# Optimization experiments

Hardware: AMD Instinct MI355X
Metric: run time of the kernel (lower is better)

Reference implementation:

```python
import jax, jax.numpy as jnp
import numpy as np
import math

DIM = 1024
HEADS = 16
DH = DIM // HEADS
HIDDEN = 4 * DIM
B, N = 2, 1024
DT = 0.05


def _cplx(r, i):
    return jax.lax.complex(r, i)


def clin(x, Wr, Wi, br, bi):
    # complex linear: (xr + i xi)(Wr + i Wi)^T + (br + i bi)
    xr, xi = x.real, x.imag
    real = xr @ Wr.T - xi @ Wi.T + br
    imag = xr @ Wi.T + xi @ Wr.T + bi
    return _cplx(real, imag)


def setup_inputs() -> dict:
    key = jax.random.key(0)
    ks = jax.random.split(key, 32)
    s = 0.02
    d = {
        'x_real': jax.random.normal(ks[0], (B, N, DIM), jnp.float32),
        'x_imag': jax.random.normal(ks[1], (B, N, DIM), jnp.float32),
    }
    i = 2
    for name in ['q', 'k', 'v', 'o']:
        d[f'Wr_{name}'] = jax.random.normal(ks[i], (DIM, DIM), jnp.float32) * s; i += 1
        d[f'Wi_{name}'] = jax.random.normal(ks[i], (DIM, DIM), jnp.float32) * s; i += 1
        d[f'br_{name}'] = jnp.zeros((DIM,), jnp.float32)
        d[f'bi_{name}'] = jnp.zeros((DIM,), jnp.float32)
    d['Wr_f1'] = jax.random.normal(ks[i], (HIDDEN, DIM), jnp.float32) * s; i += 1
    d['Wi_f1'] = jax.random.normal(ks[i], (HIDDEN, DIM), jnp.float32) * s; i += 1
    d['br_f1'] = jnp.zeros((HIDDEN,), jnp.float32)
    d['bi_f1'] = jnp.zeros((HIDDEN,), jnp.float32)
    d['Wr_f2'] = jax.random.normal(ks[i], (DIM, HIDDEN), jnp.float32) * s; i += 1
    d['Wi_f2'] = jax.random.normal(ks[i], (DIM, HIDDEN), jnp.float32) * s; i += 1
    d['br_f2'] = jnp.zeros((DIM,), jnp.float32)
    d['bi_f2'] = jnp.zeros((DIM,), jnp.float32)
    H0 = jax.random.normal(ks[i], (DIM, DIM), jnp.float32) * s; i += 1
    d['H'] = (H0 + H0.T) / 2
    d['dt'] = jnp.float32(DT)
    return d


def _forward(x_real, x_imag,
             Wr_q, Wi_q, br_q, bi_q, Wr_k, Wi_k, br_k, bi_k,
             Wr_v, Wi_v, br_v, bi_v, Wr_o, Wi_o, br_o, bi_o,
             Wr_f1, Wi_f1, br_f1, bi_f1, Wr_f2, Wi_f2, br_f2, bi_f2,
             H, dt):
    x = _cplx(x_real, x_imag)  # [B,N,D] complex64
    scale = 1.0 / math.sqrt(DH)

    # --- Quantum Fourier attention ---
    def heads(t):
        return t.reshape(B, N, HEADS, DH).transpose(0, 2, 1, 3)  # [B,H,N,dh]
    Q = heads(clin(x, Wr_q, Wi_q, br_q, bi_q))
    K = heads(clin(x, Wr_k, Wi_k, br_k, bi_k))
    V = heads(clin(x, Wr_v, Wi_v, br_v, bi_v))
    Qf = jnp.fft.fft(Q, axis=2)
    Kf = jnp.fft.fft(K, axis=2)
    Vf = jnp.fft.fft(V, axis=2)
    scores = jnp.einsum('bhid,bhjd->bhij', Qf, jnp.conj(Kf)) * scale
    attn = jax.nn.softmax(scores.real, axis=-1).astype(jnp.complex64)
    out_f = jnp.einsum('bhij,bhjd->bhid', attn, Vf)
    out = jnp.fft.ifft(out_f, axis=2).transpose(0, 2, 1, 3).reshape(B, N, DIM)
    attn_out = clin(out, Wr_o, Wi_o, br_o, bi_o)
    x = x + attn_out

    # --- Quantum feed-forward (GELU on real & imag separately, exact erf) ---
    h = clin(x, Wr_f1, Wi_f1, br_f1, bi_f1)
    h = _cplx(jax.nn.gelu(h.real, approximate=False),
              jax.nn.gelu(h.imag, approximate=False))
    x = x + clin(h, Wr_f2, Wi_f2, br_f2, bi_f2)

    # --- Schrodinger unitary evolution: U = expm(-i H dt) ---
    A = _cplx(jnp.zeros_like(H), -(H * dt))  # complex64
    U = jax.scipy.linalg.expm(A)
    out = (x.reshape(B * N, DIM) @ U).reshape(B, N, DIM)
    return out


def reference(x_real, x_imag,
              Wr_q, Wi_q, br_q, bi_q, Wr_k, Wi_k, br_k, bi_k,
              Wr_v, Wi_v, br_v, bi_v, Wr_o, Wi_o, br_o, bi_o,
              Wr_f1, Wi_f1, br_f1, bi_f1, Wr_f2, Wi_f2, br_f2, bi_f2,
              H, dt):
    out = _forward(x_real, x_imag,
                   Wr_q, Wi_q, br_q, bi_q, Wr_k, Wi_k, br_k, bi_k,
                   Wr_v, Wi_v, br_v, bi_v, Wr_o, Wi_o, br_o, bi_o,
                   Wr_f1, Wi_f1, br_f1, bi_f1, Wr_f2, Wi_f2, br_f2, bi_f2,
                   H, dt)
    # return real/imag stacked for easy real-valued comparison: [2,B,N,D]
    return jnp.stack([out.real, out.imag], axis=0)
```

## Files before the change

### kernel.cpp

```cpp
#include <hip/hip_runtime.h>
#include <cstdint>
#include <cstddef>

typedef unsigned int u32;
typedef unsigned short u16;
typedef long long i64;

typedef __attribute__((ext_vector_type(8))) short short8;
typedef __attribute__((ext_vector_type(4))) float f32x4;
typedef __attribute__((ext_vector_type(4))) int i32x4;

__device__ __forceinline__ u16 f2bf(float f) {
  u32 u = __float_as_uint(f);
  u = (u + 0x7FFFu + ((u >> 16) & 1u)) >> 16;
  return (u16)u;
}
__device__ __forceinline__ float bf2f(u16 h) { return __uint_as_float(((u32)h) << 16); }

__device__ __forceinline__ short8 neg8(short8 v) {
  i32x4 u = __builtin_bit_cast(i32x4, v);
  u = u ^ (int)0x80008000u;
  return __builtin_bit_cast(short8, u);
}
__device__ __forceinline__ f32x4 mfma16(short8 a, short8 b, f32x4 c) {
  return __builtin_amdgcn_mfma_f32_16x16x32_bf16(a, b, c, 0, 0, 0);
}
__device__ __forceinline__ float gelu_f(float x) {
  return 0.5f * x * (1.0f + erff(x * 0.7071067811865475f));
}
__device__ __forceinline__ void gl16(const u16* g, u16* l) {
  __builtin_amdgcn_global_load_lds((const __attribute__((address_space(1))) void*)g,
                                   (__attribute__((address_space(3))) void*)l, 16, 0, 0);
}
template <int N>
__device__ __forceinline__ void wait_barrier() {
  asm volatile("s_waitcnt vmcnt(%0)\n\ts_barrier" ::"i"(N) : "memory");
}

struct GemmP {
  const u16 *Arh, *Aih, *Arl, *Ail;
  const u16 *Brh, *Bih, *Brl, *Bil;
  const float *biasr, *biasi;
  const float *Resr, *Resi;
  float *Cr32, *Ci32;
  u16 *Crh, *Cih, *Crl, *Cil;
  i64 sA1, sA2, sB1, sB2, sC1, sC2;
  int ZH;
  int M, N, K, lda, ldb, ldc;
  float alpha;
  int beta, wb32, ctrans, bias_mode, bias_period, gelu, splitB;
  float bias_scale;
};

template <int CMODE, int SPLIT, int DEEP>
__global__ __launch_bounds__(256, 2) void cgemm_kernel(GemmP p) {
  constexpr int BUFU = SPLIT ? 24576 : 12288;
  constexpr int NBUF = DEEP ? 3 : 1;
  __shared__ u16 smem[BUFU * NBUF];
  constexpr bool HAS_CI = (CMODE == 0 || CMODE == 2 || CMODE == 3);
  constexpr bool AI = (CMODE == 0 || CMODE == 3);
  constexpr bool BIc = (CMODE == 0 || CMODE == 2 || CMODE == 3);
  constexpr int LPS = 3 + (AI ? 2 : 0) + (BIc ? 1 : 0);

  const int tid = threadIdx.x, lane = tid & 63, wave = tid >> 6;
  const int lrow = lane & 15, quad = lane >> 4;
  const int m0 = blockIdx.y * 128, n0 = blockIdx.x * 64;
  const int z1 = blockIdx.z / p.ZH, z2 = blockIdx.z % p.ZH;
  const i64 zA = (i64)z1 * p.sA1 + (i64)z2 * p.sA2;
  const i64 zB = (i64)z1 * p.sB1 + (i64)z2 * p.sB2;
  const i64 zC = (i64)z1 * p.sC1 + (i64)z2 * p.sC2;
  const int l4 = lane >> 2;
  const int lc = DEEP ? ((((lane & 3) ^ ((lane >> 3) & 3))) << 3) : ((lane & 3) << 3);
  const i64 aoff0 = zA + (i64)(m0 + 32 * wave + l4) * p.lda + lc;
  const i64 aoff1 = aoff0 + (i64)16 * p.lda;
  const i64 boff = zB + (i64)(n0 + 16 * wave + l4) * p.ldb + lc;
  const int lA0 = (32 * wave) * 32, lA1 = lA0 + 512;
  const int lB0 = (16 * wave) * 32;
  const int cxw = ((lrow >> 1) & 3) << 3;

  f32x4 accR[2][4], accI[2][4];
  const f32x4 z4 = {0.f, 0.f, 0.f, 0.f};
#pragma unroll
  for (int i = 0; i < 2; ++i)
#pragma unroll
    for (int j = 0; j < 4; ++j) { accR[i][j] = z4; accI[i][j] = z4; }

  const int ktn = p.K >> 5;

  if constexpr (SPLIT && !DEEP) {
    for (int kt = 0; kt < ktn; ++kt) {
      const i64 kc = (i64)(kt << 5);
      __syncthreads();
      gl16(p.Arh + aoff0 + kc, smem + lA0);
      gl16(p.Arh + aoff1 + kc, smem + lA1);
      gl16(p.Aih + aoff0 + kc, smem + 4096 + lA0);
      gl16(p.Aih + aoff1 + kc, smem + 4096 + lA1);
      gl16(p.Arl + aoff0 + kc, smem + 8192 + lA0);
      gl16(p.Arl + aoff1 + kc, smem + 8192 + lA1);
      gl16(p.Ail + aoff0 + kc, smem + 12288 + lA0);
      gl16(p.Ail + aoff1 + kc, smem + 12288 + lA1);
      gl16(p.Brh + boff + kc, smem + 16384 + lB0);
      gl16(p.Bih + boff + kc, smem + 18432 + lB0);
      if (p.splitB) {
        gl16(p.Brl + boff + kc, smem + 20480 + lB0);
        gl16(p.Bil + boff + kc, smem + 22528 + lB0);
      }
      __syncthreads();

      short8 bRh[4], bIh[4], bRl[4], bIl[4];
#pragma unroll
      for (int j = 0; j < 4; ++j) {
        const int off = (j * 16 + lrow) * 32 + quad * 8;
        bRh[j] = *(const short8*)&smem[16384 + off];
        bIh[j] = *(const short8*)&smem[18432 + off];
        if (p.splitB) {
          bRl[j] = *(const short8*)&smem[20480 + off];
          bIl[j] = *(const short8*)&smem[22528 + off];
        }
      }
#pragma unroll
      for (int i = 0; i < 2; ++i) {
        const int off = (wave * 32 + i * 16 + lrow) * 32 + quad * 8;
        short8 aRh = *(const short8*)&smem[off];
        short8 aIh = *(const short8*)&smem[4096 + off];
        short8 aRl = *(const short8*)&smem[8192 + off];
        short8 aIl = *(const short8*)&smem[12288 + off];
        if constexpr (CMODE == 0) {
          short8 nIh = neg8(aIh), nIl = neg8(aIl);
#pragma unroll
          for (int j = 0; j < 4; ++j) {
            accR[i][j] = mfma16(aRh, bRh[j], accR[i][j]);
            accR[i][j] = mfma16(nIh, bIh[j], accR[i][j]);
            accI[i][j] = mfma16(aRh, bIh[j], accI[i][j]);
            accI[i][j] = mfma16(aIh, bRh[j], accI[i][j]);
            accR[i][j] = mfma16(aRl, bRh[j], accR[i][j]);
            accR[i][j] = mfma16(nIl, bIh[j], accR[i][j]);
            accI[i][j] = mfma16(aRl, bIh[j], accI[i][j]);
            accI[i][j] = mfma16(aIl, bRh[j], accI[i][j]);
            if (p.splitB) {
              accR[i][j] = mfma16(aRh, bRl[j], accR[i][j]);
              accR[i][j] = mfma16(nIh, bIl[j], accR[i][j]);
              accI[i][j] = mfma16(aRh, bIl[j], accI[i][j]);
              accI[i][j] = mfma16(aIh, bRl[j], accI[i][j]);
            }
          }
        } else {
#pragma unroll
          for (int j = 0; j < 4; ++j) {
            accR[i][j] = mfma16(aRh, bRh[j], accR[i][j]);
            accR[i][j] = mfma16(aIh, bIh[j], accR[i][j]);
            accR[i][j] = mfma16(aRl, bRh[j], accR[i][j]);
            accR[i][j] = mfma16(aIl, bIh[j], accR[i][j]);
            accR[i][j] = mfma16(aRh, bRl[j], accR[i][j]);
            accR[i][j] = mfma16(aIh, bIl[j], accR[i][j]);
          }
        }
      }
    }
  } else if constexpr (SPLIT && DEEP) {
    auto stageS = [&](int buf, i64 kc) {
      u16* s = smem + buf * 24576;
      gl16(p.Arh + aoff0 + kc, s + lA0);
      gl16(p.Arh + aoff1 + kc, s + lA1);
      gl16(p.Aih + aoff0 + kc, s + 4096 + lA0);
      gl16(p.Aih + aoff1 + kc, s + 4096 + lA1);
      gl16(p.Arl + aoff0 + kc, s + 8192 + lA0);
      gl16(p.Arl + aoff1 + kc, s + 8192 + lA1);
      gl16(p.Ail + aoff0 + kc, s + 12288 + lA0);
      gl16(p.Ail + aoff1 + kc, s + 12288 + lA1);
      gl16(p.Brh + boff + kc, s + 16384 + lB0);
      gl16(p.Bih + boff + kc, s + 18432 + lB0);
      if (p.splitB) {
        gl16(p.Brl + boff + kc, s + 20480 + lB0);
        gl16(p.Bil + boff + kc, s + 22528 + lB0);
      }
    };
    if (ktn > 0) stageS(0, 0);
    if (ktn > 1) stageS(1, 32);
    for (int kt = 0; kt < ktn; ++kt) {
      if (kt + 1 < ktn) {
        if (p.splitB) wait_barrier<12>(); else wait_barrier<10>();
      } else {
        wait_barrier<0>();
      }
      if (kt + 2 < ktn) stageS((kt + 2) % 3, (i64)((kt + 2) << 5));
      const u16* sb = smem + (kt % 3) * 24576;

      short8 bRh[4], bIh[4], bRl[4], bIl[4];
#pragma unroll
      for (int j = 0; j < 4; ++j) {
        const int off = (j * 16 + lrow) * 32 + (quad * 8 ^ cxw);
        bRh[j] = *(const short8*)&sb[16384 + off];
        bIh[j] = *(const short8*)&sb[18432 + off];
        if (p.splitB) {
          bRl[j] = *(const short8*)&sb[20480 + off];
          bIl[j] = *(const short8*)&sb[22528 + off];
        }
      }
#pragma unroll
      for (int i = 0; i < 2; ++i) {
        const int off = (wave * 32 + i * 16 + lrow) * 32 + (quad * 8 ^ cxw);
        short8 aRh = *(const short8*)&sb[off];
        short8 aIh = *(const short8*)&sb[4096 + off];
        short8 aRl = *(const short8*)&sb[8192 + off];
        short8 aIl = *(const short8*)&sb[12288 + off];
        if constexpr (CMODE == 0) {
          short8 nIh = neg8(aIh), nIl = neg8(aIl);
#pragma unroll
          for (int j = 0; j < 4; ++j) {
            accR[i][j] = mfma16(aRh, bRh[j], accR[i][j]);
            accR[i][j] = mfma16(nIh, bIh[j], accR[i][j]);
            accI[i][j] = mfma16(aRh, bIh[j], accI[i][j]);
            accI[i][j] = mfma16(aIh, bRh[j], accI[i][j]);
            accR[i][j] = mfma16(aRl, bRh[j], accR[i][j]);
            accR[i][j] = mfma16(nIl, bIh[j], accR[i][j]);
            accI[i][j] = mfma16(aRl, bIh[j], accI[i][j]);
            accI[i][j] = mfma16(aIl, bRh[j], accI[i][j]);
            if (p.splitB) {
              accR[i][j] = mfma16(aRh, bRl[j], accR[i][j]);
              accR[i][j] = mfma16(nIh, bIl[j], accR[i][j]);
              accI[i][j] = mfma16(aRh, bIl[j], accI[i][j]);
              accI[i][j] = mfma16(aIh, bRl[j], accI[i][j]);
            }
          }
        } else {
#pragma unroll
          for (int j = 0; j < 4; ++j) {
            accR[i][j] = mfma16(aRh, bRh[j], accR[i][j]);
            accR[i][j] = mfma16(aIh, bIh[j], accR[i][j]);
            accR[i][j] = mfma16(aRl, bRh[j], accR[i][j]);
            accR[i][j] = mfma16(aIl, bIh[j], accR[i][j]);
            accR[i][j] = mfma16(aRh, bRl[j], accR[i][j]);
            accR[i][j] = mfma16(aIh, bIl[j], accR[i][j]);
          }
        }
      }
    }
  } else {
    auto stage = [&](int buf, i64 kc) {
      u16* s = smem + buf * 12288;
      gl16(p.Arh + aoff0 + kc, s + lA0);
      gl16(p.Arh + aoff1 + kc, s + lA1);
      if constexpr (AI) {
        gl16(p.Aih + aoff0 + kc, s + 4096 + lA0);
        gl16(p.Aih + aoff1 + kc, s + 4096 + lA1);
      }
      gl16(p.Brh + boff + kc, s + 8192 + lB0);
      if constexpr (BIc) gl16(p.Bih + boff + kc, s + 10240 + lB0);
    };
    if (ktn > 0) stage(0, 0);
    if (ktn > 1) stage(1, 32);
    for (int kt = 0; kt < ktn; ++kt) {
      if (kt + 1 < ktn) wait_barrier<LPS>(); else wait_barrier<0>();
      if (kt + 2 < ktn) stage((kt + 2) % 3, (i64)((kt + 2) << 5));
      const u16* sb = smem + (kt % 3) * 12288;

      short8 bR[4], bI[4];
#pragma unroll
      for (int j = 0; j < 4; ++j) {
        const int off = (j * 16 + lrow) * 32 + (quad * 8 ^ cxw);
        bR[j] = *(const short8*)&sb[8192 + off];
        if constexpr (BIc) bI[j] = *(const short8*)&sb[10240 + off];
      }
#pragma unroll
      for (int i = 0; i < 2; ++i) {
        const int off = (wave * 32 + i * 16 + lrow) * 32 + (quad * 8 ^ cxw);
        short8 aR = *(const short8*)&sb[off];
        if constexpr (CMODE == 0) {
          short8 aI = *(const short8*)&sb[4096 + off];
          short8 nI = neg8(aI);
#pragma unroll
          for (int j = 0; j < 4; ++j) {
            accR[i][j] = mfma16(aR, bR[j], accR[i][j]);
            accR[i][j] = mfma16(nI, bI[j], accR[i][j]);
            accI[i][j] = mfma16(aR, bI[j], accI[i][j]);
            accI[i][j] = mfma16(aI, bR[j], accI[i][j]);
          }
        } else if constexpr (CMODE == 1) {
#pragma unroll
          for (int j = 0; j < 4; ++j) accR[i][j] = mfma16(aR, bR[j], accR[i][j]);
        } else if constexpr (CMODE == 2) {
#pragma unroll
          for (int j = 0; j < 4; ++j) {
            accR[i][j] = mfma16(aR, bR[j], accR[i][j]);
            accI[i][j] = mfma16(aR, bI[j], accI[i][j]);
          }
        } else {
          short8 aI = *(const short8*)&sb[4096 + off];
          short8 nI = neg8(aI);
#pragma unroll
          for (int j = 0; j < 4; ++j) {
            accR[i][j] = mfma16(aR, bR[j], accR[i][j]);
            accR[i][j] = mfma16(aI, bI[j], accR[i][j]);
            accI[i][j] = mfma16(aR, bI[j], accI[i][j]);
            accI[i][j] = mfma16(nI, bR[j], accI[i][j]);
          }
        }
      }
    }
  }

#pragma unroll
  for (int i = 0; i < 2; ++i) {
#pragma unroll
    for (int j = 0; j < 4; ++j) {
      const int gn = n0 + j * 16 + lrow;
#pragma unroll
      for (int r = 0; r < 4; ++r) {
        const int gm = m0 + wave * 32 + i * 16 + quad * 4 + r;
        const i64 idx = p.ctrans ? (zC + (i64)gn * p.ldc + gm) : (zC + (i64)gm * p.ldc + gn);
        float vr = accR[i][j][r] * p.alpha;
        float vi = 0.f;
        if (HAS_CI) vi = accI[i][j][r] * p.alpha;
        if (p.beta) {
          vr += p.Cr32[idx];
          if (HAS_CI && p.Ci32) vi += p.Ci32[idx];
        }
        if (p.bias_mode == 1) {
          vr += p.biasr[gn];
          if (HAS_CI) vi += p.biasi[gn];
        } else if (p.bias_mode == 2) {
          if ((gm % p.bias_period) == 0) {
            vr += p.biasr[gn] * p.bias_scale;
            if (HAS_CI) vi += p.biasi[gn] * p.bias_scale;
          }
        }
        if (p.Resr) vr += p.Resr[idx];
        if (HAS_CI && p.Resi) vi += p.Resi[idx];
        if (p.gelu) {
          vr = gelu_f(vr);
          if (HAS_CI) vi = gelu_f(vi);
        }
        if (p.wb32 && p.Cr32) p.Cr32[idx] = vr;
        if (p.wb32 && HAS_CI && p.Ci32) p.Ci32[idx] = vi;
        if (p.Crh) {
          const u16 hh = f2bf(vr);
          p.Crh[idx] = hh;
          if (p.Crl) p.Crl[idx] = f2bf(vr - bf2f(hh));
        }
        if (HAS_CI && p.Cih) {
          const u16 hh = f2bf(vi);
          p.Cih[idx] = hh;
          if (p.Cil) p.Cil[idx] = f2bf(vi - bf2f(hh));
        }
      }
    }
  }
}

struct CvtBatch {
  const float* src[12];
  u16* hi[12];
  u16* lo[12];
  i64 cum[13];
};
__global__ __launch_bounds__(256) void cvt_batch_kernel(CvtBatch b) {
  const i64 k = (i64)blockIdx.x * 1024 + (i64)threadIdx.x * 4;
  int s = 0;
  while (k >= b.cum[s + 1]) ++s;
  const i64 base = k - b.cum[s];
  float4 v = *(const float4*)(b.src[s] + base);
  u16* hp = b.hi[s];
  u16* lp = b.lo[s];
  ushort4 h, l;
  h.x = f2bf(v.x); l.x = f2bf(v.x - bf2f(h.x));
  h.y = f2bf(v.y); l.y = f2bf(v.y - bf2f(h.y));
  h.z = f2bf(v.z); l.z = f2bf(v.z - bf2f(h.z));
  h.w = f2bf(v.w); l.w = f2bf(v.w - bf2f(h.w));
  *(ushort4*)(hp + base) = h;
  if (lp) *(ushort4*)(lp + base) = l;
}

__global__ __launch_bounds__(256) void cvt_split_kernel(const float* in, u16* hi, u16* lo,
                                                        i64 n, const float* scale_ptr) {
  const i64 base = (i64)blockIdx.x * 1024 + (i64)threadIdx.x * 4;
  const float s = scale_ptr ? *scale_ptr : 1.0f;
#pragma unroll
  for (int e = 0; e < 4; ++e) {
    const i64 k = base + e;
    if (k < n) {
      const float v = in[k] * s;
      const u16 h = f2bf(v);
      hi[k] = h;
      if (lo) lo[k] = f2bf(v - bf2f(h));
    }
  }
}

__global__ __launch_bounds__(256) void trans_cvt_kernel(const float* in, u16* outh, u16* outl) {
  __shared__ float t[32][33];
  const int b = blockIdx.z;
  const int j0 = blockIdx.y * 32;
  const int d0 = blockIdx.x * 32;
  const int r = threadIdx.x >> 5, c = threadIdx.x & 31;
  const float* ip = in + (i64)b * 1048576;
#pragma unroll
  for (int it = 0; it < 4; ++it) t[r + it * 8][c] = ip[(i64)(j0 + r + it * 8) * 1024 + d0 + c];
  __syncthreads();
  u16* ohp = outh + (i64)b * 1048576;
  u16* olp = outl + (i64)b * 1048576;
#pragma unroll
  for (int it = 0; it < 4; ++it) {
    const float v = t[c][r + it * 8];
    const i64 o = (i64)(d0 + r + it * 8) * 1024 + j0 + c;
    const u16 h = f2bf(v);
    ohp[o] = h;
    olp[o] = f2bf(v - bf2f(h));
  }
}

__global__ __launch_bounds__(256) void gen_F_kernel(u16* Frh, u16* Frl, u16* Fih, u16* Fil) {
  const int idx = blockIdx.x * 256 + threadIdx.x;
  const int mm = idx >> 10, kk = idx & 1023;
  const int t = (mm * kk) & 1023;
  float sv, cv;
  sincosf((float)t * 6.135923151e-3f, &sv, &cv);
  const float fr = cv, fi = -sv;
  u16 h = f2bf(fr);
  Frh[idx] = h;
  Frl[idx] = f2bf(fr - bf2f(h));
  h = f2bf(fi);
  Fih[idx] = h;
  Fil[idx] = f2bf(fi - bf2f(h));
}

__global__ __launch_bounds__(256) void assemble_U_kernel(const float* X2m, const float* Hm,
                                                         const float* dtp, u16* Urh, u16* Uih) {
  const int idx = blockIdx.x * 256 + threadIdx.x;
  const int i = idx >> 10, j = idx & 1023;
  const float dt = *dtp;
  const float ur = ((i == j) ? 1.0f : 0.0f) - 0.5f * X2m[idx];
  const float ui = -dt * Hm[idx];
  Urh[idx] = f2bf(ur);
  Uih[idx] = f2bf(ui);
}

__global__ __launch_bounds__(256) void softmax_kernel(float* S) {
  float* row = S + (i64)blockIdx.x * 1024;
  const int t = threadIdx.x;
  float4 v = *(float4*)(row + t * 4);
  float m = fmaxf(fmaxf(v.x, v.y), fmaxf(v.z, v.w));
#pragma unroll
  for (int off = 32; off > 0; off >>= 1) m = fmaxf(m, __shfl_down(m, off));
  __shared__ float red[8];
  const int lane = t & 63, w = t >> 6;
  if (lane == 0) red[w] = m;
  __syncthreads();
  if (t == 0) red[4] = fmaxf(fmaxf(red[0], red[1]), fmaxf(red[2], red[3]));
  __syncthreads();
  m = red[4];
  v.x = expf(v.x - m);
  v.y = expf(v.y - m);
  v.z = expf(v.z - m);
  v.w = expf(v.w - m);
  float s = v.x + v.y + v.z + v.w;
#pragma unroll
  for (int off = 32; off > 0; off >>= 1) s += __shfl_down(s, off);
  if (lane == 0) red[w] = s;
  __syncthreads();
  if (t == 0) red[5] = red[0] + red[1] + red[2] + red[3];
  __syncthreads();
  const float inv = 1.0f / red[5];
  ushort4 o;
  o.x = f2bf(v.x * inv);
  o.y = f2bf(v.y * inv);
  o.z = f2bf(v.z * inv);
  o.w = f2bf(v.w * inv);
  *(ushort4*)((u16*)row + t * 4) = o;
}

static void run_gemm(hipStream_t s, int cmode, int split, int deep, const GemmP& p, int Z) {
  dim3 g((unsigned)(p.N >> 6), (unsigned)(p.M >> 7), (unsigned)Z);
  dim3 b(256, 1, 1);
  if (split) {
    if (deep) hipLaunchKernelGGL(HIP_KERNEL_NAME(cgemm_kernel<0, 1, 1>), g, b, 0, s, p);
    else hipLaunchKernelGGL(HIP_KERNEL_NAME(cgemm_kernel<1, 1, 0>), g, b, 0, s, p);
  } else {
    if (cmode == 0) hipLaunchKernelGGL(HIP_KERNEL_NAME(cgemm_kernel<0, 0, 1>), g, b, 0, s, p);
    else if (cmode == 1) hipLaunchKernelGGL(HIP_KERNEL_NAME(cgemm_kernel<1, 0, 1>), g, b, 0, s, p);
    else if (cmode == 2) hipLaunchKernelGGL(HIP_KERNEL_NAME(cgemm_kernel<2, 0, 1>), g, b, 0, s, p);
    else hipLaunchKernelGGL(HIP_KERNEL_NAME(cgemm_kernel<3, 0, 1>), g, b, 0, s, p);
  }
}

extern "C" void kernel_launch(void* const* d_in, const int* in_sizes, int n_in, void* d_out,
                              int out_size, void* d_ws, size_t ws_size, hipStream_t stream) {
  (void)in_sizes; (void)n_in; (void)out_size; (void)ws_size;
  const float* x_real = (const float*)d_in[0];
  const float* x_imag = (const float*)d_in[1];
  const float* Wr_q = (const float*)d_in[2];
  const float* Wi_q = (const float*)d_in[3];
  const float* br_q = (const float*)d_in[4];
  const float* bi_q = (const float*)d_in[5];
  const float* Wr_k = (const float*)d_in[6];
  const float* Wi_k = (const float*)d_in[7];
  const float* br_k = (const float*)d_in[8];
  const float* bi_k = (const float*)d_in[9];
  const float* Wr_v = (const float*)d_in[10];
  const float* Wi_v = (const float*)d_in[11];
  const float* br_v = (const float*)d_in[12];
  const float* bi_v = (const float*)d_in[13];
  const float* Wr_o = (const float*)d_in[14];
  const float* Wi_o = (const float*)d_in[15];
  const float* br_o = (const float*)d_in[16];
  const float* bi_o = (const float*)d_in[17];
  const float* Wr_f1 = (const float*)d_in[18];
  const float* Wi_f1 = (const float*)d_in[19];
  const float* br_f1 = (const float*)d_in[20];
  const float* bi_f1 = (const float*)d_in[21];
  const float* Wr_f2 = (const float*)d_in[22];
  const float* Wi_f2 = (const float*)d_in[23];
  const float* br_f2 = (const float*)d_in[24];
  const float* bi_f2 = (const float*)d_in[25];
  const float* Hm = (const float*)d_in[26];
  const float* dtp = (const float*)d_in[27];

  const size_t MBy = 1ull << 20;
  char* W = (char*)d_ws;
  auto U16 = [&](size_t mb) { return (u16*)(W + mb * MBy); };
  auto F32p = [&](size_t mb) { return (float*)(W + mb * MBy); };

  float* scores = F32p(0);
  u16 *xT_rh = U16(0), *xT_ih = U16(4), *xT_rl = U16(8), *xT_il = U16(12);
  u16 *Wq_rh = U16(16), *Wq_ih = U16(18), *Wq_rl = U16(20), *Wq_il = U16(22);
  u16 *Wk_rh = U16(24), *Wk_ih = U16(26), *Wk_rl = U16(28), *Wk_il = U16(30);
  u16 *xf_rh = U16(32), *xf_ih = U16(36), *xf_rl = U16(40), *xf_il = U16(44);
  u16 *h_r = U16(64), *h_i = U16(80);
  u16 *x2_rh = U16(96), *x2_ih = U16(100), *x2_rl = U16(104), *x2_il = U16(108);
  u16* Xh = U16(112);
  float* X2m = F32p(114);
  u16 *Urh = U16(124), *Uih = U16(126);
  u16 *Wv_rh = U16(128), *Wv_ih = U16(130);
  u16 *Wo_rh = U16(132), *Wo_ih = U16(134);
  u16 *Wf1_rh = U16(136), *Wf1_ih = U16(144);
  u16 *Wf2_rh = U16(152), *Wf2_ih = U16(160);
  u16 *F_rh = U16(168), *F_ih = U16(170), *F_rl = U16(172), *F_il = U16(174);
  u16 *Qf_rh = U16(176), *Qf_ih = U16(180), *Qf_rl = U16(184), *Qf_il = U16(188);
  u16 *Kf_rh = U16(192), *Kf_ih = U16(196), *Kf_rl = U16(200), *Kf_il = U16(204);
  u16 *VfT_r = U16(208), *VfT_i = U16(212);
  u16 *ofT_r = U16(216), *ofT_i = U16(220);
  u16 *ot_r = U16(224), *ot_i = U16(228);
  float* x1_r = F32p(232);
  float* x1_i = F32p(240);
  u16 *x1h_r = U16(248), *x1h_i = U16(252);

  {
    CvtBatch b{};
    const float* srcs[12] = {Wr_q, Wi_q, Wr_k, Wi_k, Wr_v, Wi_v, Wr_o, Wi_o,
                             Wr_f1, Wi_f1, Wr_f2, Wi_f2};
    u16* his[12] = {Wq_rh, Wq_ih, Wk_rh, Wk_ih, Wv_rh, Wv_ih, Wo_rh, Wo_ih,
                    Wf1_rh, Wf1_ih, Wf2_rh, Wf2_ih};
    u16* los[12] = {Wq_rl, Wq_il, Wk_rl, Wk_il, nullptr, nullptr, nullptr, nullptr,
                    nullptr, nullptr, nullptr, nullptr};
    const i64 sizes[12] = {1048576, 1048576, 1048576, 1048576, 1048576, 1048576, 1048576,
                           1048576, 4194304, 4194304, 4194304, 4194304};
    i64 c = 0;
    for (int i = 0; i < 12; ++i) {
      b.src[i] = srcs[i]; b.hi[i] = his[i]; b.lo[i] = los[i];
      b.cum[i] = c; c += sizes[i];
    }
    b.cum[12] = c;
    hipLaunchKernelGGL(cvt_batch_kernel, dim3((unsigned)(c / 1024)), dim3(256), 0, stream, b);
  }
  hipLaunchKernelGGL(trans_cvt_kernel, dim3(32, 32, 2), dim3(256), 0, stream, x_real, xT_rh, xT_rl);
  hipLaunchKernelGGL(trans_cvt_kernel, dim3(32, 32, 2), dim3(256), 0, stream, x_imag, xT_ih, xT_il);
  hipLaunchKernelGGL(gen_F_kernel, dim3(4096), dim3(256), 0, stream, F_rh, F_rl, F_ih, F_il);

  GemmP p;
  auto clearp = [&]() {
    p = GemmP{};
    p.alpha = 1.0f;
    p.ZH = 1;
  };

  clearp();
  p.M = 1024; p.N = 1024; p.K = 1024; p.lda = 1024; p.ldb = 1024; p.ldc = 1024;
  p.sB1 = 1048576; p.sC1 = 1048576;
  p.Arh = F_rh; p.Aih = F_ih; p.Arl = F_rl; p.Ail = F_il;
  p.Brh = xT_rh; p.Bih = xT_ih; p.Brl = xT_rl; p.Bil = xT_il; p.splitB = 1;
  p.Crh = xf_rh; p.Cih = xf_ih; p.Crl = xf_rl; p.Cil = xf_il;
  run_gemm(stream, 0, 1, 1, p, 2);

  auto proj = [&](const u16* Wrh, const u16* Wih, const u16* Wrl, const u16* Wil,
                  const float* br, const float* bi, u16* Orh, u16* Oih, u16* Orl, u16* Oil) {
    clearp();
    p.M = 2048; p.N = 1024; p.K = 1024; p.lda = 1024; p.ldb = 1024; p.ldc = 1024;
    p.Arh = xf_rh; p.Aih = xf_ih; p.Arl = xf_rl; p.Ail = xf_il;
    p.Brh = Wrh; p.Bih = Wih; p.Brl = Wrl; p.Bil = Wil; p.splitB = 1;
    p.bias_mode = 2; p.bias_period = 1024; p.bias_scale = 1024.0f;
    p.biasr = br; p.biasi = bi;
    p.Crh = Orh; p.Cih = Oih; p.Crl = Orl; p.Cil = Oil;
    run_gemm(stream, 0, 1, 1, p, 1);
  };
  proj(Wq_rh, Wq_ih, Wq_rl, Wq_il, br_q, bi_q, Qf_rh, Qf_ih, Qf_rl, Qf_il);
  proj(Wk_rh, Wk_ih, Wk_rl, Wk_il, br_k, bi_k, Kf_rh, Kf_ih, Kf_rl, Kf_il);

  clearp();
  p.M = 1024; p.N = 1024; p.K = 1024; p.lda = 1024; p.ldb = 1024; p.ldc = 1024;
  p.sA1 = 1048576; p.sC1 = 1048576;
  p.Arh = xf_rh; p.Aih = xf_ih; p.Brh = Wv_rh; p.Bih = Wv_ih;
  p.bias_mode = 2; p.bias_period = 1024; p.bias_scale = 1024.0f;
  p.biasr = br_v; p.biasi = bi_v;
  p.ctrans = 1;
  p.Crh = VfT_r; p.Cih = VfT_i;
  run_gemm(stream, 0, 0, 1, p, 2);

  clearp();
  p.M = 1024; p.N = 1024; p.K = 64; p.lda = 1024; p.ldb = 1024; p.ldc = 1024;
  p.ZH = 16;
  p.sA1 = 1048576; p.sA2 = 64; p.sB1 = 1048576; p.sB2 = 64;
  p.sC1 = 16ll * 1048576; p.sC2 = 1048576;
  p.alpha = 0.125f;
  p.Arh = Qf_rh; p.Aih = Qf_ih; p.Arl = Qf_rl; p.Ail = Qf_il;
  p.Brh = Kf_rh; p.Bih = Kf_ih; p.Brl = Kf_rl; p.Bil = Kf_il; p.splitB = 1;
  p.Cr32 = scores; p.wb32 = 1;
  run_gemm(stream, 1, 1, 0, p, 32);

  hipLaunchKernelGGL(softmax_kernel, dim3(32768), dim3(256), 0, stream, scores);

  clearp();
  p.M = 1024; p.N = 64; p.K = 1024; p.lda = 2048; p.ldb = 1024; p.ldc = 1024;
  p.ZH = 16;
  p.sA1 = 16ll * 2097152; p.sA2 = 2097152;
  p.sB1 = 1048576; p.sB2 = 65536;
  p.sC1 = 1048576; p.sC2 = 65536;
  p.ctrans = 1;
  p.Arh = (const u16*)scores; p.Brh = VfT_r; p.Bih = VfT_i;
  p.Crh = ofT_r; p.Cih = ofT_i;
  run_gemm(stream, 2, 0, 1, p, 32);

  clearp();
  p.M = 1024; p.N = 1024; p.K = 1024; p.lda = 1024; p.ldb = 1024; p.ldc = 1024;
  p.sB1 = 1048576; p.sC1 = 1048576;
  p.alpha = 1.0f / 1024.0f;
  p.Arh = F_rh; p.Aih = F_ih; p.Brh = ofT_r; p.Bih = ofT_i;
  p.Crh = ot_r; p.Cih = ot_i;
  run_gemm(stream, 3, 0, 1, p, 2);

  clearp();
  p.M = 2048; p.N = 1024; p.K = 1024; p.lda = 1024; p.ldb = 1024; p.ldc = 1024;
  p.Arh = ot_r; p.Aih = ot_i; p.Brh = Wo_rh; p.Bih = Wo_ih;
  p.bias_mode = 1; p.biasr = br_o; p.biasi = bi_o;
  p.Resr = x_real; p.Resi = x_imag;
  p.Cr32 = x1_r; p.Ci32 = x1_i; p.wb32 = 1; p.Crh = x1h_r; p.Cih = x1h_i;
  run_gemm(stream, 0, 0, 1, p, 1);

  clearp();
  p.M = 2048; p.N = 4096; p.K = 1024; p.lda = 1024; p.ldb = 1024; p.ldc = 4096;
  p.Arh = x1h_r; p.Aih = x1h_i; p.Brh = Wf1_rh; p.Bih = Wf1_ih;
  p.bias_mode = 1; p.biasr = br_f1; p.biasi = bi_f1;
  p.gelu = 1;
  p.Crh = h_r; p.Cih = h_i;
  run_gemm(stream, 0, 0, 1, p, 1);

  clearp();
  p.M = 2048; p.N = 1024; p.K = 4096; p.lda = 4096; p.ldb = 4096; p.ldc = 1024;
  p.Arh = h_r; p.Aih = h_i; p.Brh = Wf2_rh; p.Bih = Wf2_ih;
  p.bias_mode = 1; p.biasr = br_f2; p.biasi = bi_f2;
  p.Resr = x1_r; p.Resi = x1_i;
  p.Crh = x2_rh; p.Cih = x2_ih; p.Crl = x2_rl; p.Cil = x2_il;
  run_gemm(stream, 0, 0, 1, p, 1);

  hipLaunchKernelGGL(cvt_split_kernel, dim3(1024), dim3(256), 0, stream, Hm, Xh,
                     (u16*)nullptr, (i64)1048576, dtp);

  clearp();
  p.M = 1024; p.N = 1024; p.K = 1024; p.lda = 1024; p.ldb = 1024; p.ldc = 1024;
  p.Arh = Xh; p.Brh = Xh;
  p.Cr32 = X2m; p.wb32 = 1;
  run_gemm(stream, 1, 0, 1, p, 1);
  hipLaunchKernelGGL(assemble_U_kernel, dim3(4096), dim3(256), 0, stream, X2m, Hm, dtp, Urh, Uih);

  float* out_r = (float*)d_out;
  float* out_i = out_r + 2097152;
  clearp();
  p.M = 2048; p.N = 1024; p.K = 1024; p.lda = 1024; p.ldb = 1024; p.ldc = 1024;
  p.Arh = x2_rh; p.Aih = x2_ih; p.Arl = x2_rl; p.Ail = x2_il;
  p.Brh = Urh; p.Bih = Uih; p.splitB = 0;
  p.Cr32 = out_r; p.Ci32 = out_i; p.wb32 = 1;
  run_gemm(stream, 0, 1, 1, p, 1);
}
```

Measured before the change: 969.3 us.

## Load B fragments directly from global memory instead of staging through LDS

In the deep-pipelined GEMM paths, the B tiles are no longer staged into shared memory. Each wave reads its B fragments directly from global memory (relying on L1/L2 reuse), and only the A tiles stay in the triple-buffered LDS pipeline. This shrinks the LDS footprint and the wait counts, and drops LDS writes and reads for B. The cost is that all four waves issue redundant uncoalesced 16-byte global loads, and these loads are synchronously exposed right before the MFMAs with no prefetch.

```diff
diff --git a/kernel.cpp b/kernel.cpp
--- a/kernel.cpp
+++ b/kernel.cpp
@@ -54,13 +54,13 @@
 
 template <int CMODE, int SPLIT, int DEEP>
 __global__ __launch_bounds__(256, 2) void cgemm_kernel(GemmP p) {
-  constexpr int BUFU = SPLIT ? 24576 : 12288;
-  constexpr int NBUF = DEEP ? 3 : 1;
-  __shared__ u16 smem[BUFU * NBUF];
   constexpr bool HAS_CI = (CMODE == 0 || CMODE == 2 || CMODE == 3);
   constexpr bool AI = (CMODE == 0 || CMODE == 3);
   constexpr bool BIc = (CMODE == 0 || CMODE == 2 || CMODE == 3);
-  constexpr int LPS = 3 + (AI ? 2 : 0) + (BIc ? 1 : 0);
+  constexpr int BUFU = SPLIT ? (DEEP ? 16384 : 24576) : (AI ? 8192 : 4096);
+  constexpr int NBUF = DEEP ? 3 : 1;
+  __shared__ u16 smem[BUFU * NBUF];
+  constexpr int LPSA = SPLIT ? 8 : (AI ? 4 : 2);
 
   const int tid = threadIdx.x, lane = tid & 63, wave = tid >> 6;
   const int lrow = lane & 15, quad = lane >> 4;
@@ -77,6 +77,11 @@
   const int lA0 = (32 * wave) * 32, lA1 = lA0 + 512;
   const int lB0 = (16 * wave) * 32;
   const int cxw = ((lrow >> 1) & 3) << 3;
+
+  i64 bro[4];
+#pragma unroll
+  for (int j = 0; j < 4; ++j)
+    bro[j] = zB + (i64)(n0 + j * 16 + lrow) * p.ldb + quad * 8;
 
   f32x4 accR[2][4], accI[2][4];
   const f32x4 z4 = {0.f, 0.f, 0.f, 0.f};
@@ -158,8 +163,8 @@
       }
     }
   } else if constexpr (SPLIT && DEEP) {
-    auto stageS = [&](int buf, i64 kc) {
-      u16* s = smem + buf * 24576;
+    auto stageA = [&](int buf, i64 kc) {
+      u16* s = smem + buf * 16384;
       gl16(p.Arh + aoff0 + kc, s + lA0);
       gl16(p.Arh + aoff1 + kc, s + lA1);
       gl16(p.Aih + aoff0 + kc, s + 4096 + lA0);
@@ -168,35 +173,24 @@
       gl16(p.Arl + aoff1 + kc, s + 8192 + lA1);
       gl16(p.Ail + aoff0 + kc, s + 12288 + lA0);
       gl16(p.Ail + aoff1 + kc, s + 12288 + lA1);
-      gl16(p.Brh + boff + kc, s + 16384 + lB0);
-      gl16(p.Bih + boff + kc, s + 18432 + lB0);
-      if (p.splitB) {
-        gl16(p.Brl + boff + kc, s + 20480 + lB0);
-        gl16(p.Bil + boff + kc, s + 22528 + lB0);
-      }
     };
-    if (ktn > 0) stageS(0, 0);
-    if (ktn > 1) stageS(1, 32);
+    if (ktn > 0) stageA(0, 0);
+    if (ktn > 1) stageA(1, 32);
     for (int kt = 0; kt < ktn; ++kt) {
-      if (kt + 1 < ktn) {
-        if (p.splitB) wait_barrier<12>(); else wait_barrier<10>();
-      } else {
-        wait_barrier<0>();
-      }
-      if (kt + 2 < ktn) stageS((kt + 2) % 3, (i64)((kt + 2) << 5));
-      const u16* sb = smem + (kt % 3) * 24576;
-
+      if (kt + 1 < ktn) wait_barrier<LPSA>(); else wait_barrier<0>();
+      const i64 kc = (i64)(kt << 5);
       short8 bRh[4], bIh[4], bRl[4], bIl[4];
 #pragma unroll
       for (int j = 0; j < 4; ++j) {
-        const int off = (j * 16 + lrow) * 32 + (quad * 8 ^ cxw);
-        bRh[j] = *(const short8*)&sb[16384 + off];
-        bIh[j] = *(const short8*)&sb[18432 + off];
+        bRh[j] = *(const short8*)(p.Brh + bro[j] + kc);
+        bIh[j] = *(const short8*)(p.Bih + bro[j] + kc);
         if (p.splitB) {
-          bRl[j] = *(const short8*)&sb[20480 + off];
-          bIl[j] = *(const short8*)&sb[22528 + off];
-        }
-      }
+          bRl[j] = *(const short8*)(p.Brl + bro[j] + kc);
+          bIl[j] = *(const short8*)(p.Bil + bro[j] + kc);
+        }
+      }
+      if (kt + 2 < ktn) stageA((kt + 2) % 3, (i64)((kt + 2) << 5));
+      const u16* sb = smem + (kt % 3) * 16384;
 #pragma unroll
       for (int i = 0; i < 2; ++i) {
         const int off = (wave * 32 + i * 16 + lrow) * 32 + (quad * 8 ^ cxw);
@@ -237,31 +231,28 @@
       }
     }
   } else {
-    auto stage = [&](int buf, i64 kc) {
-      u16* s = smem + buf * 12288;
+    auto stageA = [&](int buf, i64 kc) {
+      u16* s = smem + buf * BUFU;
       gl16(p.Arh + aoff0 + kc, s + lA0);
       gl16(p.Arh + aoff1 + kc, s + lA1);
       if constexpr (AI) {
         gl16(p.Aih + aoff0 + kc, s + 4096 + lA0);
         gl16(p.Aih + aoff1 + kc, s + 4096 + lA1);
       }
-      gl16(p.Brh + boff + kc, s + 8192 + lB0);
-      if constexpr (BIc) gl16(p.Bih + boff + kc, s + 10240 + lB0);
     };
-    if (ktn > 0) stage(0, 0);
-    if (ktn > 1) stage(1, 32);
+    if (ktn > 0) stageA(0, 0);
+    if (ktn > 1) stageA(1, 32);
     for (int kt = 0; kt < ktn; ++kt) {
-      if (kt + 1 < ktn) wait_barrier<LPS>(); else wait_barrier<0>();
-      if (kt + 2 < ktn) stage((kt + 2) % 3, (i64)((kt + 2) << 5));
-      const u16* sb = smem + (kt % 3) * 12288;
-
+      if (kt + 1 < ktn) wait_barrier<LPSA>(); else wait_barrier<0>();
+      const i64 kc = (i64)(kt << 5);
       short8 bR[4], bI[4];
 #pragma unroll
       for (int j = 0; j < 4; ++j) {
-        const int off = (j * 16 + lrow) * 32 + (quad * 8 ^ cxw);
-        bR[j] = *(const short8*)&sb[8192 + off];
-        if constexpr (BIc) bI[j] = *(const short8*)&sb[10240 + off];
-      }
+        bR[j] = *(const short8*)(p.Brh + bro[j] + kc);
+        if constexpr (BIc) bI[j] = *(const short8*)(p.Bih + bro[j] + kc);
+      }
+      if (kt + 2 < ktn) stageA((kt + 2) % 3, (i64)((kt + 2) << 5));
+      const u16* sb = smem + (kt % 3) * BUFU;
 #pragma unroll
       for (int i = 0; i < 2; ++i) {
         const int off = (wave * 32 + i * 16 + lrow) * 32 + (quad * 8 ^ cxw);
```

Result: slower. 1.461 ms (+50.7%).

## Load B fragments directly from global into registers with double buffering

Applied to the files above, without the earlier changes.

The DEEP pipelined GEMM path no longer stages B tiles through LDS. Each lane loads its B fragments straight from global memory into registers, prefetching the next k-step while computing the current one. This shrinks shared memory per buffer and cuts LDS traffic and async-load count, but loses B reuse across the four waves, so each wave reads B from global/L2 separately and the wait counts now depend on vmem ordering.

```diff
diff --git a/kernel.cpp b/kernel.cpp
--- a/kernel.cpp
+++ b/kernel.cpp
@@ -54,13 +54,14 @@
 
 template <int CMODE, int SPLIT, int DEEP>
 __global__ __launch_bounds__(256, 2) void cgemm_kernel(GemmP p) {
-  constexpr int BUFU = SPLIT ? 24576 : 12288;
-  constexpr int NBUF = DEEP ? 3 : 1;
-  __shared__ u16 smem[BUFU * NBUF];
   constexpr bool HAS_CI = (CMODE == 0 || CMODE == 2 || CMODE == 3);
   constexpr bool AI = (CMODE == 0 || CMODE == 3);
   constexpr bool BIc = (CMODE == 0 || CMODE == 2 || CMODE == 3);
-  constexpr int LPS = 3 + (AI ? 2 : 0) + (BIc ? 1 : 0);
+  constexpr int BUFU = SPLIT ? 24576 : (AI ? 8192 : 4096);
+  constexpr int NBUF = DEEP ? 3 : 1;
+  __shared__ u16 smem[BUFU * NBUF];
+  constexpr int LPSA = AI ? 4 : 2;
+  constexpr int NB = BIc ? 8 : 4;
 
   const int tid = threadIdx.x, lane = tid & 63, wave = tid >> 6;
   const int lrow = lane & 15, quad = lane >> 4;
@@ -77,6 +78,11 @@
   const int lA0 = (32 * wave) * 32, lA1 = lA0 + 512;
   const int lB0 = (16 * wave) * 32;
   const int cxw = ((lrow >> 1) & 3) << 3;
+
+  i64 bro[4];
+#pragma unroll
+  for (int j = 0; j < 4; ++j)
+    bro[j] = zB + (i64)(n0 + j * 16 + lrow) * p.ldb + quad * 8;
 
   f32x4 accR[2][4], accI[2][4];
   const f32x4 z4 = {0.f, 0.f, 0.f, 0.f};
@@ -237,31 +243,32 @@
       }
     }
   } else {
-    auto stage = [&](int buf, i64 kc) {
-      u16* s = smem + buf * 12288;
+    auto stageA = [&](int buf, i64 kc) {
+      u16* s = smem + buf * BUFU;
       gl16(p.Arh + aoff0 + kc, s + lA0);
       gl16(p.Arh + aoff1 + kc, s + lA1);
       if constexpr (AI) {
         gl16(p.Aih + aoff0 + kc, s + 4096 + lA0);
         gl16(p.Aih + aoff1 + kc, s + 4096 + lA1);
       }
-      gl16(p.Brh + boff + kc, s + 8192 + lB0);
-      if constexpr (BIc) gl16(p.Bih + boff + kc, s + 10240 + lB0);
     };
-    if (ktn > 0) stage(0, 0);
-    if (ktn > 1) stage(1, 32);
+    short8 bCurR[4], bCurI[4], bNxtR[4], bNxtI[4];
+    auto loadB = [&](short8* br, short8* bi, i64 kc) {
+#pragma unroll
+      for (int j = 0; j < 4; ++j) {
+        br[j] = *(const short8*)(p.Brh + bro[j] + kc);
+        if constexpr (BIc) bi[j] = *(const short8*)(p.Bih + bro[j] + kc);
+      }
+    };
+    if (ktn > 0) stageA(0, 0);
+    if (ktn > 1) stageA(1, 32);
+    if (ktn > 0) loadB(bCurR, bCurI, 0);
+#pragma unroll 2
     for (int kt = 0; kt < ktn; ++kt) {
-      if (kt + 1 < ktn) wait_barrier<LPS>(); else wait_barrier<0>();
-      if (kt + 2 < ktn) stage((kt + 2) % 3, (i64)((kt + 2) << 5));
-      const u16* sb = smem + (kt % 3) * 12288;
-
-      short8 bR[4], bI[4];
-#pragma unroll
-      for (int j = 0; j < 4; ++j) {
-        const int off = (j * 16 + lrow) * 32 + (quad * 8 ^ cxw);
-        bR[j] = *(const short8*)&sb[8192 + off];
-        if constexpr (BIc) bI[j] = *(const short8*)&sb[10240 + off];
-      }
+      if (kt + 1 < ktn) wait_barrier<NB + LPSA>(); else wait_barrier<NB>();
+      if (kt + 1 < ktn) loadB(bNxtR, bNxtI, (i64)((kt + 1) << 5));
+      if (kt + 2 < ktn) stageA((kt + 2) % 3, (i64)((kt + 2) << 5));
+      const u16* sb = smem + (kt % 3) * BUFU;
 #pragma unroll
       for (int i = 0; i < 2; ++i) {
         const int off = (wave * 32 + i * 16 + lrow) * 32 + (quad * 8 ^ cxw);
@@ -271,31 +278,36 @@
           short8 nI = neg8(aI);
 #pragma unroll
           for (int j = 0; j < 4; ++j) {
-            accR[i][j] = mfma16(aR, bR[j], accR[i][j]);
-            accR[i][j] = mfma16(nI, bI[j], accR[i][j]);
-            accI[i][j] = mfma16(aR, bI[j], accI[i][j]);
-            accI[i][j] = mfma16(aI, bR[j], accI[i][j]);
+            accR[i][j] = mfma16(aR, bCurR[j], accR[i][j]);
+            accR[i][j] = mfma16(nI, bCurI[j], accR[i][j]);
+            accI[i][j] = mfma16(aR, bCurI[j], accI[i][j]);
+            accI[i][j] = mfma16(aI, bCurR[j], accI[i][j]);
           }
         } else if constexpr (CMODE == 1) {
 #pragma unroll
-          for (int j = 0; j < 4; ++j) accR[i][j] = mfma16(aR, bR[j], accR[i][j]);
+          for (int j = 0; j < 4; ++j) accR[i][j] = mfma16(aR, bCurR[j], accR[i][j]);
         } else if constexpr (CMODE == 2) {
 #pragma unroll
           for (int j = 0; j < 4; ++j) {
-            accR[i][j] = mfma16(aR, bR[j], accR[i][j]);
-            accI[i][j] = mfma16(aR, bI[j], accI[i][j]);
+            accR[i][j] = mfma16(aR, bCurR[j], accR[i][j]);
+            accI[i][j] = mfma16(aR, bCurI[j], accI[i][j]);
           }
         } else {
           short8 aI = *(const short8*)&sb[4096 + off];
           short8 nI = neg8(aI);
 #pragma unroll
           for (int j = 0; j < 4; ++j) {
-            accR[i][j] = mfma16(aR, bR[j], accR[i][j]);
-            accR[i][j] = mfma16(aI, bI[j], accR[i][j]);
-            accI[i][j] = mfma16(aR, bI[j], accI[i][j]);
-            accI[i][j] = mfma16(nI, bR[j], accI[i][j]);
-          }
-        }
+            accR[i][j] = mfma16(aR, bCurR[j], accR[i][j]);
+            accR[i][j] = mfma16(aI, bCurI[j], accR[i][j]);
+            accI[i][j] = mfma16(aR, bCurI[j], accI[i][j]);
+            accI[i][j] = mfma16(nI, bCurR[j], accI[i][j]);
+          }
+        }
+      }
+#pragma unroll
+      for (int j = 0; j < 4; ++j) {
+        bCurR[j] = bNxtR[j];
+        if constexpr (BIc) bCurI[j] = bNxtI[j];
       }
     }
   }
```

After: 1.315 ms. 35.6% more time.

## Shrink non-split GEMM tile to 64x64 with 2x2 wave layout

Applied to the files above, without the earlier changes.

For the non-split complex GEMM path, the block tile goes from 128x64 to 64x64, with waves arranged 2x2, each computing a 32x32 sub-tile. Shared memory per stage shrinks and the load count per stage is adjusted. The grid doubles along M, which raises the block count and occupancy for the smaller GEMMs (attention per-head, FFT-sized products). The cost is lower data reuse per block and more global traffic for B.

```diff
diff --git a/kernel.cpp b/kernel.cpp
--- a/kernel.cpp
+++ b/kernel.cpp
@@ -54,36 +54,39 @@
 
 template <int CMODE, int SPLIT, int DEEP>
 __global__ __launch_bounds__(256, 2) void cgemm_kernel(GemmP p) {
-  constexpr int BUFU = SPLIT ? 24576 : 12288;
-  constexpr int NBUF = DEEP ? 3 : 1;
-  __shared__ u16 smem[BUFU * NBUF];
   constexpr bool HAS_CI = (CMODE == 0 || CMODE == 2 || CMODE == 3);
   constexpr bool AI = (CMODE == 0 || CMODE == 3);
   constexpr bool BIc = (CMODE == 0 || CMODE == 2 || CMODE == 3);
-  constexpr int LPS = 3 + (AI ? 2 : 0) + (BIc ? 1 : 0);
+  constexpr int BUFU = SPLIT ? 24576 : 8192;
+  constexpr int NBUF = DEEP ? 3 : 1;
+  __shared__ u16 smem[BUFU * NBUF];
+  constexpr int LPS64 = 2 + (AI ? 1 : 0) + (BIc ? 1 : 0);
+  constexpr int NJ = SPLIT ? 4 : 2;
 
   const int tid = threadIdx.x, lane = tid & 63, wave = tid >> 6;
   const int lrow = lane & 15, quad = lane >> 4;
-  const int m0 = blockIdx.y * 128, n0 = blockIdx.x * 64;
+  const int wr = wave >> 1, wc = wave & 1;
+  const int m0 = blockIdx.y * (SPLIT ? 128 : 64);
+  const int n0 = blockIdx.x * 64;
   const int z1 = blockIdx.z / p.ZH, z2 = blockIdx.z % p.ZH;
   const i64 zA = (i64)z1 * p.sA1 + (i64)z2 * p.sA2;
   const i64 zB = (i64)z1 * p.sB1 + (i64)z2 * p.sB2;
   const i64 zC = (i64)z1 * p.sC1 + (i64)z2 * p.sC2;
   const int l4 = lane >> 2;
   const int lc = DEEP ? ((((lane & 3) ^ ((lane >> 3) & 3))) << 3) : ((lane & 3) << 3);
-  const i64 aoff0 = zA + (i64)(m0 + 32 * wave + l4) * p.lda + lc;
+  const i64 aoff0 = zA + (i64)(m0 + (SPLIT ? 32 : 16) * wave + l4) * p.lda + lc;
   const i64 aoff1 = aoff0 + (i64)16 * p.lda;
   const i64 boff = zB + (i64)(n0 + 16 * wave + l4) * p.ldb + lc;
-  const int lA0 = (32 * wave) * 32, lA1 = lA0 + 512;
-  const int lB0 = (16 * wave) * 32;
+  const int lA0 = (SPLIT ? 1024 : 512) * wave, lA1 = lA0 + 512;
+  const int lB0 = 512 * wave;
   const int cxw = ((lrow >> 1) & 3) << 3;
 
-  f32x4 accR[2][4], accI[2][4];
+  f32x4 accR[2][NJ], accI[2][NJ];
   const f32x4 z4 = {0.f, 0.f, 0.f, 0.f};
 #pragma unroll
   for (int i = 0; i < 2; ++i)
 #pragma unroll
-    for (int j = 0; j < 4; ++j) { accR[i][j] = z4; accI[i][j] = z4; }
+    for (int j = 0; j < NJ; ++j) { accR[i][j] = z4; accI[i][j] = z4; }
 
   const int ktn = p.K >> 5;
 
@@ -238,39 +241,35 @@
     }
   } else {
     auto stage = [&](int buf, i64 kc) {
-      u16* s = smem + buf * 12288;
+      u16* s = smem + buf * 8192;
       gl16(p.Arh + aoff0 + kc, s + lA0);
-      gl16(p.Arh + aoff1 + kc, s + lA1);
-      if constexpr (AI) {
-        gl16(p.Aih + aoff0 + kc, s + 4096 + lA0);
-        gl16(p.Aih + aoff1 + kc, s + 4096 + lA1);
-      }
-      gl16(p.Brh + boff + kc, s + 8192 + lB0);
-      if constexpr (BIc) gl16(p.Bih + boff + kc, s + 10240 + lB0);
+      if constexpr (AI) gl16(p.Aih + aoff0 + kc, s + 2048 + lA0);
+      gl16(p.Brh + boff + kc, s + 4096 + lB0);
+      if constexpr (BIc) gl16(p.Bih + boff + kc, s + 6144 + lB0);
     };
     if (ktn > 0) stage(0, 0);
     if (ktn > 1) stage(1, 32);
     for (int kt = 0; kt < ktn; ++kt) {
-      if (kt + 1 < ktn) wait_barrier<LPS>(); else wait_barrier<0>();
+      if (kt + 1 < ktn) wait_barrier<LPS64>(); else wait_barrier<0>();
       if (kt + 2 < ktn) stage((kt + 2) % 3, (i64)((kt + 2) << 5));
-      const u16* sb = smem + (kt % 3) * 12288;
-
-      short8 bR[4], bI[4];
-#pragma unroll
-      for (int j = 0; j < 4; ++j) {
-        const int off = (j * 16 + lrow) * 32 + (quad * 8 ^ cxw);
-        bR[j] = *(const short8*)&sb[8192 + off];
-        if constexpr (BIc) bI[j] = *(const short8*)&sb[10240 + off];
+      const u16* sb = smem + (kt % 3) * 8192;
+
+      short8 bR[2], bI[2];
+#pragma unroll
+      for (int j = 0; j < 2; ++j) {
+        const int off = 4096 + (wc * 32 + j * 16 + lrow) * 32 + (quad * 8 ^ cxw);
+        bR[j] = *(const short8*)&sb[off];
+        if constexpr (BIc) bI[j] = *(const short8*)&sb[off + 2048];
       }
 #pragma unroll
       for (int i = 0; i < 2; ++i) {
-        const int off = (wave * 32 + i * 16 + lrow) * 32 + (quad * 8 ^ cxw);
+        const int off = (wr * 32 + i * 16 + lrow) * 32 + (quad * 8 ^ cxw);
         short8 aR = *(const short8*)&sb[off];
         if constexpr (CMODE == 0) {
-          short8 aI = *(const short8*)&sb[4096 + off];
+          short8 aI = *(const short8*)&sb[off + 2048];
           short8 nI = neg8(aI);
 #pragma unroll
-          for (int j = 0; j < 4; ++j) {
+          for (int j = 0; j < 2; ++j) {
             accR[i][j] = mfma16(aR, bR[j], accR[i][j]);
             accR[i][j] = mfma16(nI, bI[j], accR[i][j]);
             accI[i][j] = mfma16(aR, bI[j], accI[i][j]);
@@ -278,18 +277,18 @@
           }
         } else if constexpr (CMODE == 1) {
 #pragma unroll
-          for (int j = 0; j < 4; ++j) accR[i][j] = mfma16(aR, bR[j], accR[i][j]);
+          for (int j = 0; j < 2; ++j) accR[i][j] = mfma16(aR, bR[j], accR[i][j]);
         } else if constexpr (CMODE == 2) {
 #pragma unroll
-          for (int j = 0; j < 4; ++j) {
+          for (int j = 0; j < 2; ++j) {
             accR[i][j] = mfma16(aR, bR[j], accR[i][j]);
             accI[i][j] = mfma16(aR, bI[j], accI[i][j]);
           }
         } else {
-          short8 aI = *(const short8*)&sb[4096 + off];
+          short8 aI = *(const short8*)&sb[off + 2048];
           short8 nI = neg8(aI);
 #pragma unroll
-          for (int j = 0; j < 4; ++j) {
+          for (int j = 0; j < 2; ++j) {
             accR[i][j] = mfma16(aR, bR[j], accR[i][j]);
             accR[i][j] = mfma16(aI, bI[j], accR[i][j]);
             accI[i][j] = mfma16(aR, bI[j], accI[i][j]);
@@ -303,11 +302,12 @@
 #pragma unroll
   for (int i = 0; i < 2; ++i) {
 #pragma unroll
-    for (int j = 0; j < 4; ++j) {
-      const int gn = n0 + j * 16 + lrow;
+    for (int j = 0; j < NJ; ++j) {
+      const int gn = SPLIT ? (n0 + j * 16 + lrow) : (n0 + wc * 32 + j * 16 + lrow);
 #pragma unroll
       for (int r = 0; r < 4; ++r) {
-        const int gm = m0 + wave * 32 + i * 16 + quad * 4 + r;
+        const int gm = SPLIT ? (m0 + wave * 32 + i * 16 + quad * 4 + r)
+                             : (m0 + wr * 32 + i * 16 + quad * 4 + r);
         const i64 idx = p.ctrans ? (zC + (i64)gn * p.ldc + gm) : (zC + (i64)gm * p.ldc + gn);
         float vr = accR[i][j][r] * p.alpha;
         float vi = 0.f;
@@ -470,7 +470,7 @@
 }
 
 static void run_gemm(hipStream_t s, int cmode, int split, int deep, const GemmP& p, int Z) {
-  dim3 g((unsigned)(p.N >> 6), (unsigned)(p.M >> 7), (unsigned)Z);
+  dim3 g((unsigned)(p.N >> 6), (unsigned)(p.M >> (split ? 7 : 6)), (unsigned)Z);
   dim3 b(256, 1, 1);
   if (split) {
     if (deep) hipLaunchKernelGGL(HIP_KERNEL_NAME(cgemm_kernel<0, 1, 1>), g, b, 0, s, p);
```

New measurement: 909.4 us. 6.2% less time.
